# Kernel tuning notes

Measured on AMD Instinct MI355X. Metric: run time of the kernel, lower is better.

The kernel has to match this reference:

```python
import jax, jax.numpy as jnp
import numpy as np
from jax.scipy.linalg import expm

D_LOGIC = 128
D_MEM = 16
SO_DIM = D_MEM * (D_MEM - 1) // 2  # 120


def _linear_init(key, fan_in, shape):
    bound = 1.0 / np.sqrt(fan_in)
    return jax.random.uniform(key, shape, jnp.float32, -bound, bound)


def setup_inputs() -> dict:
    key = jax.random.key(0)
    ks = jax.random.split(key, 14)
    B, S = 4, 128
    return {
        "x_logic": jax.random.normal(ks[0], (B, S, D_LOGIC), jnp.float32),
        "x_memory": jax.random.normal(ks[1], (B, S, D_MEM), jnp.float32),
        # W_Q / W_K
        "Wq": _linear_init(ks[2], D_LOGIC, (D_LOGIC, D_LOGIC)),
        "bq": _linear_init(ks[3], D_LOGIC, (D_LOGIC,)),
        "Wk": _linear_init(ks[4], D_LOGIC, (D_LOGIC, D_LOGIC)),
        "bk": _linear_init(ks[5], D_LOGIC, (D_LOGIC,)),
        # gamma_net: Linear(d_logic, 2*d_logic) -> Tanh -> Linear(2*d_logic, so_dim)
        "W1": _linear_init(ks[6], D_LOGIC, (2 * D_LOGIC, D_LOGIC)),
        "b1": _linear_init(ks[7], D_LOGIC, (2 * D_LOGIC,)),
        "W2": _linear_init(ks[8], 2 * D_LOGIC, (SO_DIM, 2 * D_LOGIC)),
        "b2": _linear_init(ks[9], 2 * D_LOGIC, (SO_DIM,)),
        # out_proj: Linear(d_memory, d_memory)
        "Wo": _linear_init(ks[10], D_MEM, (D_MEM, D_MEM)),
        "bo": _linear_init(ks[11], D_MEM, (D_MEM,)),
    }


def reference(x_logic, x_memory, Wq, bq, Wk, bk, W1, b1, W2, b2, Wo, bo):
    B, S, d_logic = x_logic.shape
    dm = x_memory.shape[-1]

    # attention over logic stream
    Q = x_logic @ Wq.T + bq
    K = x_logic @ Wk.T + bk
    attn = jax.nn.softmax(
        jnp.einsum("bjd,bid->bji", Q, K) / jnp.sqrt(jnp.float32(d_logic)), axis=-1
    )  # [B, S(j), S(i)]

    # per-pair Lie-algebra params: delta[b,j,i] = x_logic[b,j] - x_logic[b,i]
    delta = x_logic[:, :, None, :] - x_logic[:, None, :, :]  # [B,S,S,d_logic]
    h = jnp.tanh(delta @ W1.T + b1)
    lie = h @ W2.T + b2  # [B,S,S,so_dim]

    # scatter into skew-symmetric matrices [B,S,S,dm,dm]
    r, c = np.triu_indices(dm, k=1)
    skew = jnp.zeros((B, S, S, dm, dm), x_logic.dtype)
    skew = skew.at[..., r, c].set(lie)
    skew = skew.at[..., c, r].set(-lie)

    # Lie-group exponential -> orthogonal transport matrices
    T_all = expm(skew)  # [B,S,S,dm,dm]

    # transported[b,j,i,:] = T[b,j,i] @ x_memory[b,i]
    transported = jnp.einsum("bjide,bie->bjid", T_all, x_memory)

    # attention-weighted aggregation over i
    settled = jnp.einsum("bji,bjid->bjd", attn, transported)  # [B,S,dm]

    out = settled @ Wo.T + bo
    return out, T_all
```

## Files before the change

kernel.cpp:

```cpp
#include <hip/hip_runtime.h>
#include <hip/hip_fp16.h>

#define S_LEN 128
#define DLOG  128
#define DMEM  16
#define SO    120
#define HDIM  256

typedef _Float16 v8h __attribute__((ext_vector_type(8)));
typedef __fp16 v2hf __attribute__((ext_vector_type(2)));
typedef float v4f __attribute__((ext_vector_type(4)));

union PkU { v2hf h; unsigned u; };
union V8U { v8h v; int u[4]; };

__device__ __forceinline__ v8h splat8(float x) {
  _Float16 h = (_Float16)x;
  v8h v = {h, h, h, h, h, h, h, h};
  return v;
}

__global__ __launch_bounds__(512) void qku_kernel(
    const float* __restrict__ xl, const float* __restrict__ Wq,
    const float* __restrict__ bq, const float* __restrict__ Wk,
    const float* __restrict__ bk, const float* __restrict__ W1,
    float* __restrict__ Q, float* __restrict__ K, float* __restrict__ u) {
  int bj = blockIdx.x, t = threadIdx.x;
  int lane = t & 63, wu = t >> 6;
  int half = lane >> 5, l5 = lane & 31;
  float4 xv = *(const float4*)(xl + bj * 128 + 4 * l5);
  int seg = wu >> 1;
  const float* wb;
  if (seg == 0) wb = Wq;
  else if (seg == 1) wb = Wk - 128 * 128;
  else wb = W1 - 256 * 128;
  #pragma unroll 4
  for (int step = 0; step < 32; ++step) {
    int ro = wu * 64 + 2 * step + half;
    float4 wv = *(const float4*)(wb + ro * 128 + 4 * l5);
    float v = fmaf(wv.x, xv.x, fmaf(wv.y, xv.y, fmaf(wv.z, xv.z, wv.w * xv.w)));
    v += __shfl_xor(v, 1, 64);
    v += __shfl_xor(v, 2, 64);
    v += __shfl_xor(v, 4, 64);
    v += __shfl_xor(v, 8, 64);
    v += __shfl_xor(v, 16, 64);
    if (l5 == 0) {
      if (seg == 0) Q[bj * 128 + ro] = v + bq[ro];
      else if (seg == 1) K[bj * 128 + (ro - 128)] = v + bk[ro - 128];
      else u[bj * 256 + (ro - 256)] = v;
    }
  }
}

__global__ __launch_bounds__(256) void attn_h_kernel(
    const float* __restrict__ Q, const float* __restrict__ K,
    float* __restrict__ attn, const float* __restrict__ u,
    const float* __restrict__ b1, _Float16* __restrict__ hG) {
  int t = threadIdx.x;
  if (blockIdx.x < 256) {
    int sub = t >> 7, t128 = t & 127;
    int bj = blockIdx.x * 2 + sub, b = bj >> 7;
    int lane = t & 63, wu = (t >> 6) & 1;
    int half = lane >> 5, l5 = lane & 31;
    __shared__ float sc[2][128];
    __shared__ float red[2][128];
    float4 qv = *(const float4*)(Q + bj * 128 + 4 * l5);
    #pragma unroll 4
    for (int step = 0; step < 32; ++step) {
      int ro = wu * 64 + 2 * step + half;
      float4 kv = *(const float4*)(K + (size_t)(b * 128 + ro) * 128 + 4 * l5);
      float v = fmaf(kv.x, qv.x, fmaf(kv.y, qv.y, fmaf(kv.z, qv.z, kv.w * qv.w)));
      v += __shfl_xor(v, 1, 64);
      v += __shfl_xor(v, 2, 64);
      v += __shfl_xor(v, 4, 64);
      v += __shfl_xor(v, 8, 64);
      v += __shfl_xor(v, 16, 64);
      if (l5 == 0) sc[sub][ro] = v * 0.08838834764831845f;
    }
    __syncthreads();
    int i = t128;
    float s = sc[sub][i];
    red[sub][i] = s;
    __syncthreads();
    for (int off = 64; off; off >>= 1) {
      if (i < off) red[sub][i] = fmaxf(red[sub][i], red[sub][i + off]);
      __syncthreads();
    }
    float m = red[sub][0];
    __syncthreads();
    float e = expf(s - m);
    red[sub][i] = e;
    __syncthreads();
    for (int off = 64; off; off >>= 1) {
      if (i < off) red[sub][i] += red[sub][i + off];
      __syncthreads();
    }
    attn[(size_t)bj * 128 + i] = e / red[sub][0];
    return;
  }
  int tid = (blockIdx.x - 256) * 256 + t;
  #pragma unroll
  for (int g = 0; g < 4; ++g) {
    int unit = tid + g * 524288;
    int p = unit >> 5;
    int o0 = (unit & 31) * 8;
    int bj = p >> 7;
    int b = bj >> 7;
    int i = p & 127;
    const float* uj = u + bj * 256 + o0;
    const float* ui = u + (size_t)(b * 128 + i) * 256 + o0;
    const float* bb = b1 + o0;
    float4 j0 = *(const float4*)uj, j1 = *(const float4*)(uj + 4);
    float4 i0 = *(const float4*)ui, i1 = *(const float4*)(ui + 4);
    float4 c0 = *(const float4*)bb, c1 = *(const float4*)(bb + 4);
    float xv[8] = {j0.x - i0.x + c0.x, j0.y - i0.y + c0.y,
                   j0.z - i0.z + c0.z, j0.w - i0.w + c0.w,
                   j1.x - i1.x + c1.x, j1.y - i1.y + c1.y,
                   j1.z - i1.z + c1.z, j1.w - i1.w + c1.w};
    float rv[8];
    #pragma unroll
    for (int k = 0; k < 8; ++k) {
      float x = xv[k];
      float ax = fabsf(x);
      float e = __expf(-2.f * ax);
      float r = __fdividef(1.f - e, 1.f + e);
      rv[k] = copysignf(r, x);
    }
    V8U out;
    #pragma unroll
    for (int k = 0; k < 4; ++k) {
      PkU pu;
      pu.h = __builtin_amdgcn_cvt_pkrtz(rv[2 * k], rv[2 * k + 1]);
      out.u[k] = (int)pu.u;
    }
    *(v8h*)(hG + (size_t)p * 512 + o0) = out.v;
  }
}

__global__ __launch_bounds__(512) void lie_kernel(
    const float* __restrict__ W2g, const float* __restrict__ b2g,
    float* __restrict__ Tg) {
  __shared__ _Float16 w2t[128 * 136];
  int t = threadIdx.x, lane = t & 63;
  int wu = __builtin_amdgcn_readfirstlane(t >> 6);
  int pbase = blockIdx.x * 128 + wu * 16;
  int nn = lane & 15, q = lane >> 4;
  const _Float16* hf = (const _Float16*)Tg;

  for (int idx = t; idx < 1088; idx += 512) w2t[16320 + idx] = (_Float16)0.f;

  v4f acc[8];
  #pragma unroll
  for (int tt = 0; tt < 8; ++tt) acc[tt] = (v4f){0.f, 0.f, 0.f, 0.f};

  const _Float16* hrow = hf + (size_t)(pbase + nn) * 512;
  for (int khalf = 0; khalf < 2; ++khalf) {
    __syncthreads();
    for (int idx = t; idx < 3840; idx += 512) {
      int row = idx >> 5, c4 = (idx & 31) * 4;
      float4 v = *(const float4*)(W2g + row * 256 + khalf * 128 + c4);
      PkU a, b;
      a.h = __builtin_amdgcn_cvt_pkrtz(v.x, v.y);
      b.h = __builtin_amdgcn_cvt_pkrtz(v.z, v.w);
      uint2 pk = {a.u, b.u};
      *(uint2*)(w2t + row * 136 + c4) = pk;
    }
    __syncthreads();
    #pragma unroll
    for (int ks = 0; ks < 4; ++ks) {
      v8h ah = *(const v8h*)(hrow + khalf * 128 + ks * 32 + 8 * q);
      #pragma unroll
      for (int tt = 0; tt < 8; ++tt) {
        const v8h bf = *(const v8h*)(w2t + (16 * tt + nn) * 136 + ks * 32 + 8 * q);
        acc[tt] = __builtin_amdgcn_mfma_f32_16x16x32_f16(ah, bf, acc[tt], 0, 0, 0);
      }
    }
  }

  int rc0[8], rc1[8];
  float bbv[8];
  bool val[8];
  #pragma unroll
  for (int tt = 0; tt < 8; ++tt) {
    int n16 = 16 * tt + nn;
    val[tt] = (n16 < 120);
    float fr_ = floorf((31.0f - sqrtf(961.0f - 8.0f * (float)n16)) * 0.5f);
    int r = (int)fr_;
    int Sr = 15 * r - ((r * (r - 1)) >> 1);
    int c = n16 - Sr + r + 1;
    rc0[tt] = r * 16 + c;
    rc1[tt] = c * 16 + r;
    bbv[tt] = val[tt] ? b2g[n16] : 0.f;
  }

  _Float16* hw = (_Float16*)Tg;
  _Float16* aSt = w2t;
  for (int pass = 0; pass < 2; ++pass) {
    __syncthreads();
    #pragma unroll
    for (int reg = 0; reg < 4; ++reg) {
      int pidx = 4 * q + reg;
      if ((pidx >> 3) == pass) {
        _Float16* ab = aSt + (wu * 8 + (pidx & 7)) * 256;
        #pragma unroll
        for (int tt = 0; tt < 8; ++tt) {
          if (val[tt]) {
            _Float16 hv = (_Float16)(acc[tt][reg] + bbv[tt]);
            ab[rc0[tt]] = hv;
            ab[rc1[tt]] = -hv;
          }
        }
        ab[nn * 17] = (_Float16)0.f;
      }
    }
    __syncthreads();
    #pragma unroll
    for (int k = 0; k < 4; ++k) {
      int unit = t + k * 512;
      int lp = unit >> 5, off = (unit & 31) * 8;
      int g = blockIdx.x * 128 + (lp >> 3) * 16 + pass * 8 + (lp & 7);
      *(v8h*)(hw + (size_t)g * 512 + 256 + off) = *(const v8h*)(aSt + lp * 256 + off);
    }
  }
}

__device__ __forceinline__ void split8(const float* x, v8h& hi, v8h& lo) {
  union U { v8h v; v2hf p[4]; } H, L;
  #pragma unroll
  for (int i = 0; i < 4; ++i) {
    float a = x[2 * i], b = x[2 * i + 1];
    v2hf h = __builtin_amdgcn_cvt_pkrtz(a, b);
    float ra = (float)h[0], rb = (float)h[1];
    v2hf l = __builtin_amdgcn_cvt_pkrtz(a - ra, b - rb);
    H.p[i] = h;
    L.p[i] = l;
  }
  hi = H.v;
  lo = L.v;
}

__global__ __launch_bounds__(256) void expm_kernel(
    float* __restrict__ Tg, const float* __restrict__ attn,
    const float* __restrict__ xm, float* __restrict__ part) {
  __shared__ char lds[10240] __attribute__((aligned(16)));
  __shared__ float sred[4][16];
  int t = threadIdx.x, lane = t & 63;
  int wu = __builtin_amdgcn_readfirstlane(t >> 6);
  int pbase = blockIdx.x * 8 + wu * 2;
  int nn = lane & 15, q = lane >> 4, b8 = (q & 1) * 8;
  float* ErB = (float*)(lds + wu * 2560);
  const _Float16* hf = (const _Float16*)Tg;

  int idxA = ((2 * (q & 1)) * 16 + nn) * 4;
  int idxB = idxA + 64;

  float scv[2];
  int sv[2];
  V8U Apk[2], BfA[2];
  v4f Af[2];
  #pragma unroll
  for (int j = 0; j < 2; ++j) {
    size_t p = (size_t)(pbase + j);
    const _Float16* Ap = hf + p * 512 + 256;
    v8h rowh = *(const v8h*)(Ap + nn * 16 + b8);
    float s2 = 0.f, s1 = 0.f;
    #pragma unroll
    for (int k = 0; k < 8; ++k) {
      float xf = (float)rowh[k];
      s2 = fmaf(xf, xf, s2);
      s1 += fabsf(xf);
    }
    s1 += __shfl_xor(s1, 16, 64);
    s1 = fmaxf(s1, __shfl_xor(s1, 1, 64));
    s1 = fmaxf(s1, __shfl_xor(s1, 2, 64));
    s1 = fmaxf(s1, __shfl_xor(s1, 4, 64));
    s1 = fmaxf(s1, __shfl_xor(s1, 8, 64));
    #pragma unroll
    for (int off = 1; off < 64; off <<= 1) s2 += __shfl_xor(s2, off, 64);
    float bound = fminf(0.5f * sqrtf(s2), s1);
    int s = 0;
    while (bound > 1.0f && s < 12) { bound *= 0.5f; s++; }
    sv[j] = __builtin_amdgcn_readfirstlane(s);
    scv[j] = ldexpf(1.0f, -s);
    v8h sch = splat8(scv[j]);
    V8U ap;
    ap.v = rowh * sch;
    #pragma unroll
    for (int i = 0; i < 4; ++i) {
      Apk[j].u[i] = ap.u[i];
      BfA[j].u[i] = ap.u[i] ^ 0x80008000;
    }
    #pragma unroll
    for (int reg = 0; reg < 4; ++reg)
      Af[j][reg] = (float)Ap[(4 * q + reg) * 16 + nn] * scv[j];
  }

  V8U IC1, IC2;
  #pragma unroll
  for (int i = 0; i < 4; ++i) {
    float d0 = (b8 + 2 * i == nn) ? 1.f : 0.f;
    float d1 = (b8 + 2 * i + 1 == nn) ? 1.f : 0.f;
    PkU u1, u2;
    u1.h = __builtin_amdgcn_cvt_pkrtz(10.666667f * d0, 10.666667f * d1);
    u2.h = __builtin_amdgcn_cvt_pkrtz(2.1333333f * d0, 2.1333333f * d1);
    IC1.u[i] = (int)u1.u;
    IC2.u[i] = (int)u2.u;
  }

  v4f z4 = {0.f, 0.f, 0.f, 0.f};

  v4f cB[2];
  #pragma unroll
  for (int j = 0; j < 2; ++j)
    cB[j] = __builtin_amdgcn_mfma_f32_16x16x32_f16(Apk[j].v, BfA[j].v, z4, 0, 0, 0);

  V8U fB[2];
  #pragma unroll
  for (int j = 0; j < 2; ++j) {
    PkU u0, u1;
    u0.h = __builtin_amdgcn_cvt_pkrtz(cB[j][0], cB[j][1]);
    u1.h = __builtin_amdgcn_cvt_pkrtz(cB[j][2], cB[j][3]);
    fB[j].u[0] = __builtin_amdgcn_ds_bpermute(idxA, (int)u0.u);
    fB[j].u[1] = __builtin_amdgcn_ds_bpermute(idxA, (int)u1.u);
    fB[j].u[2] = __builtin_amdgcn_ds_bpermute(idxB, (int)u0.u);
    fB[j].u[3] = __builtin_amdgcn_ds_bpermute(idxB, (int)u1.u);
  }

  v4f cB2[2];
  #pragma unroll
  for (int j = 0; j < 2; ++j)
    cB2[j] = __builtin_amdgcn_mfma_f32_16x16x32_f16(fB[j].v, fB[j].v, z4, 0, 0, 0);

  V8U fB2[2];
  #pragma unroll
  for (int j = 0; j < 2; ++j) {
    PkU u0, u1;
    u0.h = __builtin_amdgcn_cvt_pkrtz(cB2[j][0], cB2[j][1]);
    u1.h = __builtin_amdgcn_cvt_pkrtz(cB2[j][2], cB2[j][3]);
    fB2[j].u[0] = __builtin_amdgcn_ds_bpermute(idxA, (int)u0.u);
    fB2[j].u[1] = __builtin_amdgcn_ds_bpermute(idxA, (int)u1.u);
    fB2[j].u[2] = __builtin_amdgcn_ds_bpermute(idxB, (int)u0.u);
    fB2[j].u[3] = __builtin_amdgcn_ds_bpermute(idxB, (int)u1.u);
  }

  v8h k1a = splat8(7.9365079e-4f);
  v8h k1b = splat8(0.17777778f);
  v8h k2a = splat8(8.8183422e-5f);
  v8h k2b = splat8(2.5396825e-2f);
  V8U M1[2], M2[2];
  #pragma unroll
  for (int j = 0; j < 2; ++j) {
    M1[j].v = fB2[j].v * k1a + (fB[j].v * k1b + IC1.v);
    M2[j].v = fB2[j].v * k2a + (fB[j].v * k2b + IC2.v);
  }

  v4f Cc[2], Qc[2];
  #pragma unroll
  for (int j = 0; j < 2; ++j) {
    v4f c3m = __builtin_amdgcn_mfma_f32_16x16x32_f16(M1[j].v, fB2[j].v, z4, 0, 0, 0);
    v4f c4m = __builtin_amdgcn_mfma_f32_16x16x32_f16(M2[j].v, fB2[j].v, z4, 0, 0, 0);
    #pragma unroll
    for (int reg = 0; reg < 4; ++reg) {
      float dg = (4 * q + reg == nn) ? 1.f : 0.f;
      Cc[j][reg] = fmaf(c3m[reg], 2.44140625e-4f,
                        fmaf(cB[j][reg], 0.25f, dg + Af[j][reg]));
      Qc[j][reg] = fmaf(c4m[reg], 2.44140625e-4f, cB[j][reg] * 0.083333333f);
    }
  }

  V8U fQ[2];
  #pragma unroll
  for (int j = 0; j < 2; ++j) {
    PkU u0, u1;
    u0.h = __builtin_amdgcn_cvt_pkrtz(Qc[j][0], Qc[j][1]);
    u1.h = __builtin_amdgcn_cvt_pkrtz(Qc[j][2], Qc[j][3]);
    fQ[j].u[0] = __builtin_amdgcn_ds_bpermute(idxA, (int)u0.u);
    fQ[j].u[1] = __builtin_amdgcn_ds_bpermute(idxA, (int)u1.u);
    fQ[j].u[2] = __builtin_amdgcn_ds_bpermute(idxB, (int)u0.u);
    fQ[j].u[3] = __builtin_amdgcn_ds_bpermute(idxB, (int)u1.u);
  }

  v4f E[2];
  #pragma unroll
  for (int j = 0; j < 2; ++j) {
    v4f c5 = __builtin_amdgcn_mfma_f32_16x16x32_f16(Apk[j].v, fQ[j].v, z4, 0, 0, 0);
    E[j] = Cc[j] + c5 * 0.5f;
  }

  int smax = max(sv[0], sv[1]);
  for (int it = 0; it < smax; ++it) {
    #pragma unroll
    for (int j = 0; j < 2; ++j) {
      if (it < sv[j]) {
        float* Erp = ErB + j * 320;
        PkU u0, u1;
        u0.h = __builtin_amdgcn_cvt_pkrtz(E[j][0], E[j][1]);
        u1.h = __builtin_amdgcn_cvt_pkrtz(E[j][2], E[j][3]);
        V8U bfe;
        bfe.u[0] = __builtin_amdgcn_ds_bpermute(idxA, (int)u0.u);
        bfe.u[1] = __builtin_amdgcn_ds_bpermute(idxA, (int)u1.u);
        bfe.u[2] = __builtin_amdgcn_ds_bpermute(idxB, (int)u0.u);
        bfe.u[3] = __builtin_amdgcn_ds_bpermute(idxB, (int)u1.u);
        #pragma unroll
        for (int reg = 0; reg < 4; ++reg)
          Erp[(4 * q + reg) * 20 + nn] = E[j][reg];
        asm volatile("s_waitcnt lgkmcnt(0)" ::: "memory");
        float4 a0 = *(const float4*)(Erp + nn * 20 + b8);
        float4 a1 = *(const float4*)(Erp + nn * 20 + b8 + 4);
        float xa[8] = {a0.x, a0.y, a0.z, a0.w, a1.x, a1.y, a1.z, a1.w};
        v8h ahi, alo;
        split8(xa, ahi, alo);
        v8h Ecat = (q < 2) ? ahi : alo;
        v4f z = {0.f, 0.f, 0.f, 0.f};
        E[j] = __builtin_amdgcn_mfma_f32_16x16x32_f16(Ecat, bfe.v, z, 0, 0, 0);
      }
    }
  }

  float pacc[4] = {0.f, 0.f, 0.f, 0.f};
  #pragma unroll
  for (int j = 0; j < 2; ++j) {
    int p = pbase + j;
    float* dst = Tg + (size_t)p * 256;
    #pragma unroll
    for (int reg = 0; reg < 4; ++reg)
      dst[(4 * q + reg) * 16 + nn] = E[j][reg];
    int b = p >> 14, i = p & 127;
    float xv = xm[((b << 7) + i) * 16 + nn];
    float aw = attn[(size_t)p] * xv;
    #pragma unroll
    for (int reg = 0; reg < 4; ++reg)
      pacc[reg] = fmaf(aw, E[j][reg], pacc[reg]);
  }
  #pragma unroll
  for (int reg = 0; reg < 4; ++reg) {
    #pragma unroll
    for (int off = 1; off < 16; off <<= 1)
      pacc[reg] += __shfl_xor(pacc[reg], off, 64);
  }
  if (nn == 0) {
    #pragma unroll
    for (int reg = 0; reg < 4; ++reg) sred[wu][4 * q + reg] = pacc[reg];
  }
  __syncthreads();
  if (t < 16)
    part[(size_t)blockIdx.x * 16 + t] =
        sred[0][t] + sred[1][t] + sred[2][t] + sred[3][t];
}

__global__ __launch_bounds__(64) void settle_fin_kernel(
    const float* __restrict__ part, const float* __restrict__ Wo,
    const float* __restrict__ bo, float* __restrict__ outp) {
  int bj = blockIdx.x, t = threadIdx.x;
  int r = t & 15, e0 = t >> 4;
  const float* pb = part + (size_t)bj * 256;
  float s = pb[e0 * 16 + r] + pb[(e0 + 4) * 16 + r] +
            pb[(e0 + 8) * 16 + r] + pb[(e0 + 12) * 16 + r];
  __shared__ float sf[64];
  sf[t] = s;
  __syncthreads();
  if (t < 16) sf[t] = sf[t] + sf[16 + t] + sf[32 + t] + sf[48 + t];
  __syncthreads();
  if (t < 16) {
    float o = bo[t];
    const float* wr = Wo + t * 16;
    #pragma unroll
    for (int c = 0; c < 16; ++c) o = fmaf(wr[c], sf[c], o);
    outp[bj * 16 + t] = o;
  }
}

extern "C" void kernel_launch(void* const* d_in, const int* in_sizes, int n_in,
                              void* d_out, int out_size, void* d_ws,
                              size_t ws_size, hipStream_t stream) {
  const float* xl = (const float*)d_in[0];
  const float* xm = (const float*)d_in[1];
  const float* Wq = (const float*)d_in[2];
  const float* bq = (const float*)d_in[3];
  const float* Wk = (const float*)d_in[4];
  const float* bk = (const float*)d_in[5];
  const float* W1 = (const float*)d_in[6];
  const float* b1 = (const float*)d_in[7];
  const float* W2 = (const float*)d_in[8];
  const float* b2 = (const float*)d_in[9];
  const float* Wo = (const float*)d_in[10];
  const float* bo = (const float*)d_in[11];
  float* outp = (float*)d_out;
  float* Tg = outp + 8192;
  float* wsf = (float*)d_ws;
  float* Q = wsf;
  float* K = wsf + 65536;
  float* attn = wsf + 131072;
  float* u = wsf + 196608;
  float* part = wsf + 196608;

  hipLaunchKernelGGL(qku_kernel, dim3(512), dim3(512), 0, stream, xl, Wq, bq, Wk, bk, W1, Q, K, u);
  hipLaunchKernelGGL(attn_h_kernel, dim3(2304), dim3(256), 0, stream, Q, K, attn, u, b1, (_Float16*)Tg);
  hipLaunchKernelGGL(lie_kernel, dim3(512), dim3(512), 0, stream, W2, b2, Tg);
  hipLaunchKernelGGL(expm_kernel, dim3(8192), dim3(256), 0, stream, Tg, attn, xm, part);
  hipLaunchKernelGGL(settle_fin_kernel, dim3(512), dim3(64), 0, stream, part, Wo, bo, outp);
}
```

Measured before the change: 196.6 us.

## Process four expm pairs per wave and simplify the scaling-exponent computation

Each wave of expm_kernel now handles four matrix-exponential pairs instead of two. The grid is halved and settle_fin now sums 8 partials per row instead of 16. The Padé stages are interleaved per pair so more independent MFMA chains overlap and intermediate register arrays shrink. The squaring count is now read directly from the float exponent of the Frobenius bound, replacing a loop and the extra 1-norm shuffle reduction. Because that tighter min(frob, 1-norm) bound is gone, some pairs may take more squaring iterations, and the wider per-wave state raises register pressure.

After: 186.3 us. 5.2% less time.

```diff
diff --git a/kernel.cpp b/kernel.cpp
--- a/kernel.cpp
+++ b/kernel.cpp
@@ -242,54 +242,46 @@
 __global__ __launch_bounds__(256) void expm_kernel(
     float* __restrict__ Tg, const float* __restrict__ attn,
     const float* __restrict__ xm, float* __restrict__ part) {
-  __shared__ char lds[10240] __attribute__((aligned(16)));
+  __shared__ float ErB_all[4][1280];
   __shared__ float sred[4][16];
   int t = threadIdx.x, lane = t & 63;
   int wu = __builtin_amdgcn_readfirstlane(t >> 6);
-  int pbase = blockIdx.x * 8 + wu * 2;
+  int pbase = blockIdx.x * 16 + wu * 4;
   int nn = lane & 15, q = lane >> 4, b8 = (q & 1) * 8;
-  float* ErB = (float*)(lds + wu * 2560);
+  float* ErW = ErB_all[wu];
   const _Float16* hf = (const _Float16*)Tg;
 
   int idxA = ((2 * (q & 1)) * 16 + nn) * 4;
   int idxB = idxA + 64;
 
-  float scv[2];
-  int sv[2];
-  V8U Apk[2], BfA[2];
-  v4f Af[2];
-  #pragma unroll
-  for (int j = 0; j < 2; ++j) {
+  float scv[4];
+  int sv[4];
+  V8U Apk[4];
+  v4f Af[4];
+  #pragma unroll
+  for (int j = 0; j < 4; ++j) {
     size_t p = (size_t)(pbase + j);
     const _Float16* Ap = hf + p * 512 + 256;
     v8h rowh = *(const v8h*)(Ap + nn * 16 + b8);
-    float s2 = 0.f, s1 = 0.f;
+    float s2 = 0.f;
     #pragma unroll
     for (int k = 0; k < 8; ++k) {
       float xf = (float)rowh[k];
       s2 = fmaf(xf, xf, s2);
-      s1 += fabsf(xf);
-    }
-    s1 += __shfl_xor(s1, 16, 64);
-    s1 = fmaxf(s1, __shfl_xor(s1, 1, 64));
-    s1 = fmaxf(s1, __shfl_xor(s1, 2, 64));
-    s1 = fmaxf(s1, __shfl_xor(s1, 4, 64));
-    s1 = fmaxf(s1, __shfl_xor(s1, 8, 64));
+    }
     #pragma unroll
     for (int off = 1; off < 64; off <<= 1) s2 += __shfl_xor(s2, off, 64);
-    float bound = fminf(0.5f * sqrtf(s2), s1);
-    int s = 0;
-    while (bound > 1.0f && s < 12) { bound *= 0.5f; s++; }
+    float bound = 0.5f * sqrtf(s2);
+    int bb = __float_as_int(bound);
+    int s = ((bb >> 23) & 255) - 126;
+    s = min(max(s, 0), 12);
     sv[j] = __builtin_amdgcn_readfirstlane(s);
-    scv[j] = ldexpf(1.0f, -s);
+    scv[j] = __int_as_float((127 - sv[j]) << 23);
     v8h sch = splat8(scv[j]);
     V8U ap;
     ap.v = rowh * sch;
     #pragma unroll
-    for (int i = 0; i < 4; ++i) {
-      Apk[j].u[i] = ap.u[i];
-      BfA[j].u[i] = ap.u[i] ^ 0x80008000;
-    }
+    for (int i = 0; i < 4; ++i) Apk[j].u[i] = ap.u[i];
     #pragma unroll
     for (int reg = 0; reg < 4; ++reg)
       Af[j][reg] = (float)Ap[(4 * q + reg) * 16 + nn] * scv[j];
@@ -306,17 +298,24 @@
     IC1.u[i] = (int)u1.u;
     IC2.u[i] = (int)u2.u;
   }
-
+  v8h k1a = splat8(7.9365079e-4f);
+  v8h k1b = splat8(0.17777778f);
+  v8h k2a = splat8(8.8183422e-5f);
+  v8h k2b = splat8(2.5396825e-2f);
   v4f z4 = {0.f, 0.f, 0.f, 0.f};
 
-  v4f cB[2];
-  #pragma unroll
-  for (int j = 0; j < 2; ++j)
-    cB[j] = __builtin_amdgcn_mfma_f32_16x16x32_f16(Apk[j].v, BfA[j].v, z4, 0, 0, 0);
-
-  V8U fB[2];
-  #pragma unroll
-  for (int j = 0; j < 2; ++j) {
+  v4f cB[4];
+  #pragma unroll
+  for (int j = 0; j < 4; ++j) {
+    V8U bfa;
+    #pragma unroll
+    for (int i = 0; i < 4; ++i) bfa.u[i] = Apk[j].u[i] ^ 0x80008000;
+    cB[j] = __builtin_amdgcn_mfma_f32_16x16x32_f16(Apk[j].v, bfa.v, z4, 0, 0, 0);
+  }
+
+  V8U fB[4];
+  #pragma unroll
+  for (int j = 0; j < 4; ++j) {
     PkU u0, u1;
     u0.h = __builtin_amdgcn_cvt_pkrtz(cB[j][0], cB[j][1]);
     u1.h = __builtin_amdgcn_cvt_pkrtz(cB[j][2], cB[j][3]);
@@ -326,73 +325,53 @@
     fB[j].u[3] = __builtin_amdgcn_ds_bpermute(idxB, (int)u1.u);
   }
 
-  v4f cB2[2];
-  #pragma unroll
-  for (int j = 0; j < 2; ++j)
-    cB2[j] = __builtin_amdgcn_mfma_f32_16x16x32_f16(fB[j].v, fB[j].v, z4, 0, 0, 0);
-
-  V8U fB2[2];
-  #pragma unroll
-  for (int j = 0; j < 2; ++j) {
+  V8U fB2[4];
+  #pragma unroll
+  for (int j = 0; j < 4; ++j) {
+    v4f c = __builtin_amdgcn_mfma_f32_16x16x32_f16(fB[j].v, fB[j].v, z4, 0, 0, 0);
     PkU u0, u1;
-    u0.h = __builtin_amdgcn_cvt_pkrtz(cB2[j][0], cB2[j][1]);
-    u1.h = __builtin_amdgcn_cvt_pkrtz(cB2[j][2], cB2[j][3]);
+    u0.h = __builtin_amdgcn_cvt_pkrtz(c[0], c[1]);
+    u1.h = __builtin_amdgcn_cvt_pkrtz(c[2], c[3]);
     fB2[j].u[0] = __builtin_amdgcn_ds_bpermute(idxA, (int)u0.u);
     fB2[j].u[1] = __builtin_amdgcn_ds_bpermute(idxA, (int)u1.u);
     fB2[j].u[2] = __builtin_amdgcn_ds_bpermute(idxB, (int)u0.u);
     fB2[j].u[3] = __builtin_amdgcn_ds_bpermute(idxB, (int)u1.u);
   }
 
-  v8h k1a = splat8(7.9365079e-4f);
-  v8h k1b = splat8(0.17777778f);
-  v8h k2a = splat8(8.8183422e-5f);
-  v8h k2b = splat8(2.5396825e-2f);
-  V8U M1[2], M2[2];
-  #pragma unroll
-  for (int j = 0; j < 2; ++j) {
-    M1[j].v = fB2[j].v * k1a + (fB[j].v * k1b + IC1.v);
-    M2[j].v = fB2[j].v * k2a + (fB[j].v * k2b + IC2.v);
-  }
-
-  v4f Cc[2], Qc[2];
-  #pragma unroll
-  for (int j = 0; j < 2; ++j) {
-    v4f c3m = __builtin_amdgcn_mfma_f32_16x16x32_f16(M1[j].v, fB2[j].v, z4, 0, 0, 0);
-    v4f c4m = __builtin_amdgcn_mfma_f32_16x16x32_f16(M2[j].v, fB2[j].v, z4, 0, 0, 0);
+  v4f E[4];
+  #pragma unroll
+  for (int j = 0; j < 4; ++j) {
+    V8U M1, M2;
+    M1.v = fB2[j].v * k1a + (fB[j].v * k1b + IC1.v);
+    M2.v = fB2[j].v * k2a + (fB[j].v * k2b + IC2.v);
+    v4f c3m = __builtin_amdgcn_mfma_f32_16x16x32_f16(M1.v, fB2[j].v, z4, 0, 0, 0);
+    v4f c4m = __builtin_amdgcn_mfma_f32_16x16x32_f16(M2.v, fB2[j].v, z4, 0, 0, 0);
+    v4f Cc, Qc;
     #pragma unroll
     for (int reg = 0; reg < 4; ++reg) {
       float dg = (4 * q + reg == nn) ? 1.f : 0.f;
-      Cc[j][reg] = fmaf(c3m[reg], 2.44140625e-4f,
-                        fmaf(cB[j][reg], 0.25f, dg + Af[j][reg]));
-      Qc[j][reg] = fmaf(c4m[reg], 2.44140625e-4f, cB[j][reg] * 0.083333333f);
-    }
-  }
-
-  V8U fQ[2];
-  #pragma unroll
-  for (int j = 0; j < 2; ++j) {
+      Cc[reg] = fmaf(c3m[reg], 2.44140625e-4f,
+                     fmaf(cB[j][reg], 0.25f, dg + Af[j][reg]));
+      Qc[reg] = fmaf(c4m[reg], 2.44140625e-4f, cB[j][reg] * 0.083333333f);
+    }
     PkU u0, u1;
-    u0.h = __builtin_amdgcn_cvt_pkrtz(Qc[j][0], Qc[j][1]);
-    u1.h = __builtin_amdgcn_cvt_pkrtz(Qc[j][2], Qc[j][3]);
-    fQ[j].u[0] = __builtin_amdgcn_ds_bpermute(idxA, (int)u0.u);
-    fQ[j].u[1] = __builtin_amdgcn_ds_bpermute(idxA, (int)u1.u);
-    fQ[j].u[2] = __builtin_amdgcn_ds_bpermute(idxB, (int)u0.u);
-    fQ[j].u[3] = __builtin_amdgcn_ds_bpermute(idxB, (int)u1.u);
-  }
-
-  v4f E[2];
-  #pragma unroll
-  for (int j = 0; j < 2; ++j) {
-    v4f c5 = __builtin_amdgcn_mfma_f32_16x16x32_f16(Apk[j].v, fQ[j].v, z4, 0, 0, 0);
-    E[j] = Cc[j] + c5 * 0.5f;
-  }
-
-  int smax = max(sv[0], sv[1]);
+    u0.h = __builtin_amdgcn_cvt_pkrtz(Qc[0], Qc[1]);
+    u1.h = __builtin_amdgcn_cvt_pkrtz(Qc[2], Qc[3]);
+    V8U fQ;
+    fQ.u[0] = __builtin_amdgcn_ds_bpermute(idxA, (int)u0.u);
+    fQ.u[1] = __builtin_amdgcn_ds_bpermute(idxA, (int)u1.u);
+    fQ.u[2] = __builtin_amdgcn_ds_bpermute(idxB, (int)u0.u);
+    fQ.u[3] = __builtin_amdgcn_ds_bpermute(idxB, (int)u1.u);
+    v4f c5 = __builtin_amdgcn_mfma_f32_16x16x32_f16(Apk[j].v, fQ.v, z4, 0, 0, 0);
+    E[j] = Cc + c5 * 0.5f;
+  }
+
+  int smax = max(max(sv[0], sv[1]), max(sv[2], sv[3]));
   for (int it = 0; it < smax; ++it) {
     #pragma unroll
-    for (int j = 0; j < 2; ++j) {
+    for (int j = 0; j < 4; ++j) {
       if (it < sv[j]) {
-        float* Erp = ErB + j * 320;
+        float* Erp = ErW + j * 320;
         PkU u0, u1;
         u0.h = __builtin_amdgcn_cvt_pkrtz(E[j][0], E[j][1]);
         u1.h = __builtin_amdgcn_cvt_pkrtz(E[j][2], E[j][3]);
@@ -419,7 +398,7 @@
 
   float pacc[4] = {0.f, 0.f, 0.f, 0.f};
   #pragma unroll
-  for (int j = 0; j < 2; ++j) {
+  for (int j = 0; j < 4; ++j) {
     int p = pbase + j;
     float* dst = Tg + (size_t)p * 256;
     #pragma unroll
@@ -453,9 +432,8 @@
     const float* __restrict__ bo, float* __restrict__ outp) {
   int bj = blockIdx.x, t = threadIdx.x;
   int r = t & 15, e0 = t >> 4;
-  const float* pb = part + (size_t)bj * 256;
-  float s = pb[e0 * 16 + r] + pb[(e0 + 4) * 16 + r] +
-            pb[(e0 + 8) * 16 + r] + pb[(e0 + 12) * 16 + r];
+  const float* pb = part + (size_t)bj * 128;
+  float s = pb[e0 * 16 + r] + pb[(e0 + 4) * 16 + r];
   __shared__ float sf[64];
   sf[t] = s;
   __syncthreads();
@@ -497,6 +475,6 @@
   hipLaunchKernelGGL(qku_kernel, dim3(512), dim3(512), 0, stream, xl, Wq, bq, Wk, bk, W1, Q, K, u);
   hipLaunchKernelGGL(attn_h_kernel, dim3(2304), dim3(256), 0, stream, Q, K, attn, u, b1, (_Float16*)Tg);
   hipLaunchKernelGGL(lie_kernel, dim3(512), dim3(512), 0, stream, W2, b2, Tg);
-  hipLaunchKernelGGL(expm_kernel, dim3(8192), dim3(256), 0, stream, Tg, attn, xm, part);
+  hipLaunchKernelGGL(expm_kernel, dim3(4096), dim3(256), 0, stream, Tg, attn, xm, part);
   hipLaunchKernelGGL(settle_fin_kernel, dim3(512), dim3(64), 0, stream, part, Wo, bo, outp);
 }
```
